# Kernel optimization log

Hardware: AMD Instinct MI355X
Metric: run time of the kernel (lower is better)

## Reference

```python
import jax, jax.numpy as jnp
import numpy as np

SIGMA_AGG = 0.5
NUM_SEG = 33  # labels in [0, 32]; 0 = background


def setup_inputs() -> dict:
    key = jax.random.key(0)
    k1, k2, k3, k4, k5 = jax.random.split(key, 5)
    B, C, H, W = 16, 4, 736, 736
    return {
        "pred_similarities": jax.random.normal(k1, (B, C, H, W), dtype=jnp.float32),
        "regions_mask": jax.random.uniform(k2, (B, 1, H, W), dtype=jnp.float32),
        "kernels_mask": jax.random.uniform(k3, (B, 1, H, W), dtype=jnp.float32),
        "text_mask_ndi_labels": jax.random.randint(k4, (B, 1, H, W), 0, NUM_SEG, dtype=jnp.int32),
        "kernel_mask_ndi_labels": jax.random.randint(k5, (B, 1, H, W), 0, NUM_SEG, dtype=jnp.int32),
    }


def _per_batch(pred, rmask, kmask, rlab, klab):
    # pred: [C, N]; rmask/kmask: [N]; rlab/klab: [N] int
    # Per-kernel-label sum of kernels_mask, scattered back; 0 where label==0.
    ksum = jax.ops.segment_sum(kmask, klab, num_segments=NUM_SEG)            # [S]
    kcard = jnp.where(klab > 0, ksum[klab], 0.0)                              # [N]
    # Per-kernel-label sum of pred_similarities per channel.
    psum = jax.ops.segment_sum(pred.T, klab, num_segments=NUM_SEG)            # [S, C]
    Gk = jnp.where(klab[None, :] > 0, psum[klab].T, 0.0)                      # [C, N]
    # Region cardinality: faithful to source, it sums kernels_mask (not regions_mask)
    # over region labels.
    rsum = jax.ops.segment_sum(kmask, rlab, num_segments=NUM_SEG)             # [S]
    rcard = jnp.where(rlab > 0, rsum[rlab], 0.0)                              # [N]
    return kcard, Gk, rcard


def reference(pred_similarities, regions_mask, kernels_mask,
              text_mask_ndi_labels, kernel_mask_ndi_labels):
    B, C, H, W = pred_similarities.shape
    N = H * W
    pred = pred_similarities.reshape(B, C, N)
    rmask = regions_mask.reshape(B, N)
    kmask = kernels_mask.reshape(B, N)
    rlab = text_mask_ndi_labels.reshape(B, N)
    klab = kernel_mask_ndi_labels.reshape(B, N)

    kcard, Gk, rcard = jax.vmap(_per_batch)(pred, rmask, kmask, rlab, klab)
    # kcard/rcard: [B, N], Gk: [B, C, N]

    Gk = Gk / (kcard[:, None, :] + 1.0)
    Fp = pred * rmask[:, None, :]
    norm = jnp.sqrt(jnp.sum((Fp - Gk) ** 2, axis=1))                          # [B, N]
    d = jnp.maximum(norm - SIGMA_AGG, 0.0)
    D_p_K = jnp.log(d ** 2 + 1.0) / (rcard + 1.0)
    # Faithful to source bug: num_kernel is the LAST batch's max kernel label.
    num_kernel = klab[-1].max().astype(D_p_K.dtype)
    L_agg = (D_p_K / num_kernel).sum()
    return L_agg
```

## Files before the change

### kernel.cpp

```cpp
#include <hip/hip_runtime.h>


constexpr int NSEG = 33;
constexpr int NCH  = 4;
constexpr int WS_PER_B = NSEG * (NCH + 2);
constexpr int NREP = 16;
constexpr float SIGMA_AGG = 0.5f;
constexpr float QSCALE = 32768.0f;
constexpr float QINV   = 1.0f / 32768.0f;

constexpr int NUMK_OFF = 16 * WS_PER_B;
constexpr int PART_OFF = 3200;

__global__ __launch_bounds__(256) void seg_sums_kernel(
    const float* __restrict__ pred, const float* __restrict__ kmask,
    const int* __restrict__ rlab, const int* __restrict__ klab,
    int* __restrict__ ws, int* __restrict__ numk_out,
    int N, int lastB)
{
    const int b = blockIdx.y;
    __shared__ int s_acc[NREP * WS_PER_B];
    __shared__ int s_maxk;
    for (int j = threadIdx.x; j < NREP * WS_PER_B; j += blockDim.x) s_acc[j] = 0;
    if (threadIdx.x == 0) s_maxk = 0;
    __syncthreads();

    const int cbase = (threadIdx.x & (NREP - 1)) * WS_PER_B;

    const size_t bN = (size_t)b * N;
    const int Nv = N >> 2;
    const float4* __restrict__ predv = (const float4*)(pred + (size_t)b * NCH * N);
    const float4* __restrict__ kmv   = (const float4*)(kmask + bN);
    const int4*   __restrict__ rlv   = (const int4*)(rlab + bN);
    const int4*   __restrict__ klv   = (const int4*)(klab + bN);

    int mk = 0;
    for (int i = blockIdx.x * blockDim.x + threadIdx.x; i < Nv;
         i += gridDim.x * blockDim.x) {
        float4 km = kmv[i];
        int4   kl = klv[i];
        int4   rl = rlv[i];
        float4 p0 = predv[0 * Nv + i];
        float4 p1 = predv[1 * Nv + i];
        float4 p2 = predv[2 * Nv + i];
        float4 p3 = predv[3 * Nv + i];

        #define PIX(sfx) do {                                                 \
            int kl_ = kl.sfx, rl_ = rl.sfx;                                   \
            int kq = __float2int_rn(km.sfx * QSCALE);                         \
            atomicAdd(&s_acc[cbase + kl_], kq);                               \
            atomicAdd(&s_acc[cbase + NSEG + rl_], kq);                        \
            atomicAdd(&s_acc[cbase + 2 * NSEG + 0 * NSEG + kl_],              \
                      __float2int_rn(p0.sfx * QSCALE));                       \
            atomicAdd(&s_acc[cbase + 2 * NSEG + 1 * NSEG + kl_],              \
                      __float2int_rn(p1.sfx * QSCALE));                       \
            atomicAdd(&s_acc[cbase + 2 * NSEG + 2 * NSEG + kl_],              \
                      __float2int_rn(p2.sfx * QSCALE));                       \
            atomicAdd(&s_acc[cbase + 2 * NSEG + 3 * NSEG + kl_],              \
                      __float2int_rn(p3.sfx * QSCALE));                       \
            mk = max(mk, kl_);                                                \
        } while (0)
        PIX(x); PIX(y); PIX(z); PIX(w);
        #undef PIX
    }
    __syncthreads();

    int* wsb = ws + b * WS_PER_B;
    for (int j = threadIdx.x; j < WS_PER_B; j += blockDim.x) {
        int v = 0;
        #pragma unroll
        for (int r = 0; r < NREP; ++r) v += s_acc[r * WS_PER_B + j];
        atomicAdd(&wsb[j], v);
    }

    if (b == lastB) {
        atomicMax(&s_maxk, mk);
        __syncthreads();
        if (threadIdx.x == 0) atomicMax(numk_out, s_maxk);
    }
}

__global__ __launch_bounds__(256) void loss_kernel(
    const float* __restrict__ pred, const float* __restrict__ rmask,
    const int* __restrict__ rlab, const int* __restrict__ klab,
    const int* __restrict__ ws, float* __restrict__ partials, int N)
{
    const int b = blockIdx.y;
    __shared__ float s_gk[NCH * NSEG];
    __shared__ float s_rinv[NSEG];
    __shared__ float s_part[4];
    const int* wsb = ws + b * WS_PER_B;
    for (int j = threadIdx.x; j < NSEG; j += blockDim.x) {
        float rs = (float)wsb[NSEG + j] * QINV;
        s_rinv[j] = (j > 0) ? 1.0f / (rs + 1.0f) : 1.0f;
    }
    for (int j = threadIdx.x; j < NCH * NSEG; j += blockDim.x) {
        int s = j % NSEG;
        float ks = (float)wsb[s] * QINV;
        float ps = (float)wsb[2 * NSEG + j] * QINV;
        s_gk[j] = (s > 0) ? ps / (ks + 1.0f) : 0.0f;
    }
    __syncthreads();

    const size_t bN = (size_t)b * N;
    const int Nv = N >> 2;
    const float4* __restrict__ predv = (const float4*)(pred + (size_t)b * NCH * N);
    const float4* __restrict__ rmv   = (const float4*)(rmask + bN);
    const int4*   __restrict__ rlv   = (const int4*)(rlab + bN);
    const int4*   __restrict__ klv   = (const int4*)(klab + bN);

    float acc = 0.0f;
    for (int i = blockIdx.x * blockDim.x + threadIdx.x; i < Nv;
         i += gridDim.x * blockDim.x) {
        float4 rm = rmv[i];
        int4   kl = klv[i];
        int4   rl = rlv[i];
        float4 p0 = predv[0 * Nv + i];
        float4 p1 = predv[1 * Nv + i];
        float4 p2 = predv[2 * Nv + i];
        float4 p3 = predv[3 * Nv + i];

        #define PIX(sfx) do {                                        \
            int kl_ = kl.sfx, rl_ = rl.sfx; float rm_ = rm.sfx;      \
            float d0 = fmaf(p0.sfx, rm_, -s_gk[0 * NSEG + kl_]);     \
            float d1 = fmaf(p1.sfx, rm_, -s_gk[1 * NSEG + kl_]);     \
            float d2 = fmaf(p2.sfx, rm_, -s_gk[2 * NSEG + kl_]);     \
            float d3 = fmaf(p3.sfx, rm_, -s_gk[3 * NSEG + kl_]);     \
            float ss = d0*d0 + d1*d1 + d2*d2 + d3*d3;                \
            float nrm = sqrtf(ss);                                   \
            float dd = fmaxf(nrm - SIGMA_AGG, 0.0f);                 \
            acc += __logf(fmaf(dd, dd, 1.0f)) * s_rinv[rl_];         \
        } while (0)
        PIX(x); PIX(y); PIX(z); PIX(w);
        #undef PIX
    }

    for (int off = 32; off > 0; off >>= 1)
        acc += __shfl_down(acc, off);
    const int lane = threadIdx.x & 63;
    const int wid  = threadIdx.x >> 6;
    if (lane == 0) s_part[wid] = acc;
    __syncthreads();
    if (threadIdx.x == 0)
        partials[blockIdx.y * gridDim.x + blockIdx.x] =
            s_part[0] + s_part[1] + s_part[2] + s_part[3];
}

__global__ __launch_bounds__(256) void finalize_kernel(
    const float* __restrict__ partials, const int* __restrict__ numk,
    float* __restrict__ out, int nPart)
{
    __shared__ float s_part[4];
    float a = 0.0f;
    for (int i = threadIdx.x; i < nPart; i += blockDim.x) a += partials[i];
    for (int off = 32; off > 0; off >>= 1)
        a += __shfl_down(a, off);
    if ((threadIdx.x & 63) == 0) s_part[threadIdx.x >> 6] = a;
    __syncthreads();
    if (threadIdx.x == 0)
        out[0] = (s_part[0] + s_part[1] + s_part[2] + s_part[3]) / (float)(*numk);
}

extern "C" void kernel_launch(void* const* d_in, const int* in_sizes, int n_in,
                              void* d_out, int out_size, void* d_ws, size_t ws_size,
                              hipStream_t stream)
{
    const float* pred  = (const float*)d_in[0];
    const float* rmask = (const float*)d_in[1];
    const float* kmask = (const float*)d_in[2];
    const int*   rlab  = (const int*)d_in[3];
    const int*   klab  = (const int*)d_in[4];
    float* out = (float*)d_out;

    const int B = 16;
    const int N = in_sizes[1] / B;

    int* wsi = (int*)d_ws;
    int* numk = wsi + NUMK_OFF;
    float* partials = (float*)(wsi + PART_OFF);

    hipMemsetAsync(d_ws, 0, (size_t)(NUMK_OFF + 1) * sizeof(int), stream);

    dim3 block(256);
    dim3 grid(256, B);
    seg_sums_kernel<<<grid, block, 0, stream>>>(pred, kmask, rlab, klab, wsi, numk, N, B - 1);
    loss_kernel<<<grid, block, 0, stream>>>(pred, rmask, rlab, klab, wsi, partials, N);
    finalize_kernel<<<dim3(1), block, 0, stream>>>(partials, numk, out, 256 * B);
}
```

Measured before the change: 327.9 us.

## Replace shared-memory atomic histograms with per-thread private tables split by wave

```diff
diff --git a/kernel.cpp b/kernel.cpp
--- a/kernel.cpp
+++ b/kernel.cpp
@@ -4,7 +4,8 @@
 constexpr int NSEG = 33;
 constexpr int NCH  = 4;
 constexpr int WS_PER_B = NSEG * (NCH + 2);
-constexpr int NREP = 16;
+constexpr int NWAVE = 6;
+constexpr int NTHR  = NWAVE * 64;
 constexpr float SIGMA_AGG = 0.5f;
 constexpr float QSCALE = 32768.0f;
 constexpr float QINV   = 1.0f / 32768.0f;
@@ -12,71 +13,56 @@
 constexpr int NUMK_OFF = 16 * WS_PER_B;
 constexpr int PART_OFF = 3200;
 
-__global__ __launch_bounds__(256) void seg_sums_kernel(
+__global__ __launch_bounds__(NTHR) void seg_sums_kernel(
     const float* __restrict__ pred, const float* __restrict__ kmask,
     const int* __restrict__ rlab, const int* __restrict__ klab,
     int* __restrict__ ws, int* __restrict__ numk_out,
     int N, int lastB)
 {
-    const int b = blockIdx.y;
-    __shared__ int s_acc[NREP * WS_PER_B];
-    __shared__ int s_maxk;
-    for (int j = threadIdx.x; j < NREP * WS_PER_B; j += blockDim.x) s_acc[j] = 0;
-    if (threadIdx.x == 0) s_maxk = 0;
-    __syncthreads();
+    __shared__ int s_tbl[NTHR * NSEG];
+    int* mytbl = s_tbl + threadIdx.x * NSEG;
+    #pragma unroll
+    for (int j = 0; j < NSEG; ++j) mytbl[j] = 0;
 
-    const int cbase = (threadIdx.x & (NREP - 1)) * WS_PER_B;
-
+    const int b    = blockIdx.y;
+    const int wv   = threadIdx.x >> 6;
+    const int lane = threadIdx.x & 63;
     const size_t bN = (size_t)b * N;
     const int Nv = N >> 2;
-    const float4* __restrict__ predv = (const float4*)(pred + (size_t)b * NCH * N);
-    const float4* __restrict__ kmv   = (const float4*)(kmask + bN);
-    const int4*   __restrict__ rlv   = (const int4*)(rlab + bN);
-    const int4*   __restrict__ klv   = (const int4*)(klab + bN);
+
+    const float4* __restrict__ val4 =
+        (wv < 4) ? ((const float4*)(pred + (size_t)b * NCH * N)) + (size_t)wv * Nv
+                 : (const float4*)(kmask + bN);
+    const int4* __restrict__ lab4 =
+        (wv == 5) ? (const int4*)(rlab + bN) : (const int4*)(klab + bN);
 
     int mk = 0;
-    for (int i = blockIdx.x * blockDim.x + threadIdx.x; i < Nv;
-         i += gridDim.x * blockDim.x) {
-        float4 km = kmv[i];
-        int4   kl = klv[i];
-        int4   rl = rlv[i];
-        float4 p0 = predv[0 * Nv + i];
-        float4 p1 = predv[1 * Nv + i];
-        float4 p2 = predv[2 * Nv + i];
-        float4 p3 = predv[3 * Nv + i];
-
-        #define PIX(sfx) do {                                                 \
-            int kl_ = kl.sfx, rl_ = rl.sfx;                                   \
-            int kq = __float2int_rn(km.sfx * QSCALE);                         \
-            atomicAdd(&s_acc[cbase + kl_], kq);                               \
-            atomicAdd(&s_acc[cbase + NSEG + rl_], kq);                        \
-            atomicAdd(&s_acc[cbase + 2 * NSEG + 0 * NSEG + kl_],              \
-                      __float2int_rn(p0.sfx * QSCALE));                       \
-            atomicAdd(&s_acc[cbase + 2 * NSEG + 1 * NSEG + kl_],              \
-                      __float2int_rn(p1.sfx * QSCALE));                       \
-            atomicAdd(&s_acc[cbase + 2 * NSEG + 2 * NSEG + kl_],              \
-                      __float2int_rn(p2.sfx * QSCALE));                       \
-            atomicAdd(&s_acc[cbase + 2 * NSEG + 3 * NSEG + kl_],              \
-                      __float2int_rn(p3.sfx * QSCALE));                       \
-            mk = max(mk, kl_);                                                \
-        } while (0)
-        PIX(x); PIX(y); PIX(z); PIX(w);
-        #undef PIX
+    for (int u = blockIdx.x * 64 + lane; u < Nv; u += gridDim.x * 64) {
+        float4 v = val4[u];
+        int4   L = lab4[u];
+        mytbl[L.x] += __float2int_rn(v.x * QSCALE);
+        mytbl[L.y] += __float2int_rn(v.y * QSCALE);
+        mytbl[L.z] += __float2int_rn(v.z * QSCALE);
+        mytbl[L.w] += __float2int_rn(v.w * QSCALE);
+        if (wv == 4) mk = max(mk, max(max(L.x, L.y), max(L.z, L.w)));
     }
     __syncthreads();
 
-    int* wsb = ws + b * WS_PER_B;
-    for (int j = threadIdx.x; j < WS_PER_B; j += blockDim.x) {
+    if (threadIdx.x < NWAVE * NSEG) {
+        const int s = threadIdx.x / NSEG;
+        const int j = threadIdx.x - s * NSEG;
         int v = 0;
-        #pragma unroll
-        for (int r = 0; r < NREP; ++r) v += s_acc[r * WS_PER_B + j];
-        atomicAdd(&wsb[j], v);
+        #pragma unroll 8
+        for (int l = 0; l < 64; ++l) v += s_tbl[(s * 64 + l) * NSEG + j];
+        const int off = (s < 4) ? (2 * NSEG + s * NSEG + j)
+                                : ((s == 4) ? j : NSEG + j);
+        atomicAdd(&ws[b * WS_PER_B + off], v);
     }
 
-    if (b == lastB) {
-        atomicMax(&s_maxk, mk);
-        __syncthreads();
-        if (threadIdx.x == 0) atomicMax(numk_out, s_maxk);
+    if (b == lastB && wv == 4) {
+        for (int off = 32; off > 0; off >>= 1)
+            mk = max(mk, __shfl_down(mk, off));
+        if (lane == 0) atomicMax(numk_out, mk);
     }
 }
 
@@ -181,9 +167,9 @@
 
     hipMemsetAsync(d_ws, 0, (size_t)(NUMK_OFF + 1) * sizeof(int), stream);
 
-    dim3 block(256);
-    dim3 grid(256, B);
-    seg_sums_kernel<<<grid, block, 0, stream>>>(pred, kmask, rlab, klab, wsi, numk, N, B - 1);
-    loss_kernel<<<grid, block, 0, stream>>>(pred, rmask, rlab, klab, wsi, partials, N);
-    finalize_kernel<<<dim3(1), block, 0, stream>>>(partials, numk, out, 256 * B);
+    seg_sums_kernel<<<dim3(96, B), dim3(NTHR), 0, stream>>>(
+        pred, kmask, rlab, klab, wsi, numk, N, B - 1);
+    loss_kernel<<<dim3(256, B), dim3(256), 0, stream>>>(
+        pred, rmask, rlab, klab, wsi, partials, N);
+    finalize_kernel<<<dim3(1), dim3(256), 0, stream>>>(partials, numk, out, 256 * B);
 }
```

New measurement: 326.9 us. About the same (-0.3%).
